# Optimization experiments

Measured on AMD Instinct MI355X. Metric: run time of the kernel, lower is better.

## Reference

```python
import jax, jax.numpy as jnp
import numpy as np

# Model hyperparameters (match init_kwargs)
K = 4          # number of experts (branches)
STEPS = 3
TOP_N = 2
HEADS = 2
DIM_HEAD = 64
ROUTE_TEMP = 1.5
C = 256        # channels


def conv3x3(x, w, b):
    # x: [B,H,W,Cin], w: [3,3,Cin,Cout], b: [Cout]
    y = jax.lax.conv_general_dilated(
        x, w, window_strides=(1, 1), padding='SAME',
        dimension_numbers=('NHWC', 'HWIO', 'NHWC'))
    return y + b


def setup_inputs() -> dict:
    key = jax.random.key(0)
    ks = jax.random.split(key, 8)
    B, H, W = 32, 32, 32
    D = HEADS * DIM_HEAD  # 128
    glorot = jax.nn.initializers.glorot_uniform()
    x = jax.random.normal(ks[0], (B, H, W, C), dtype=jnp.float32)
    q = glorot(ks[1], (HEADS, DIM_HEAD), jnp.float32)          # router queries
    Wk = glorot(ks[2], (C, D), jnp.float32)                    # 1x1 conv key proj
    Wv = glorot(ks[3], (C, D), jnp.float32)                    # 1x1 conv val proj
    Wmlp = glorot(ks[4], (D, K), jnp.float32)                  # head_mlp (mlp_hidden=0)
    alpha = jnp.zeros((), jnp.float32)                         # attn_log_alpha
    We = glorot(ks[5], (K * 3, 3, C, C), jnp.float32).reshape(K, 3, 3, C, C)
    be = jnp.zeros((K, C), jnp.float32)
    return {"x": x, "q": q, "Wk": Wk, "Wv": Wv, "Wmlp": Wmlp,
            "alpha": alpha, "We": We, "be": be}


def reference(x, q, Wk, Wv, Wmlp, alpha, We, be):
    B, H, W, Cc = x.shape
    S = H * W
    allowed = jnp.ones((B, K), x.dtype)
    last_oh = jax.nn.one_hot(jnp.full((B,), K - 1), K, dtype=x.dtype)
    scale = jnp.asarray(S, x.dtype)
    a = jax.nn.softplus(alpha)

    for t in range(STEPS):
        # ---- AttnPoolRouter ----
        k = jnp.einsum('bhwc,cd->bhwd', x, Wk).reshape(B, S, HEADS, DIM_HEAD)
        v = jnp.einsum('bhwc,cd->bhwd', x, Wv).reshape(B, S, HEADS, DIM_HEAD)
        # attention logits: [B, heads, S]
        attn = jax.nn.softmax(
            jnp.einsum('nd,bsnd->bns', q, k) / jnp.sqrt(jnp.asarray(DIM_HEAD, x.dtype)),
            axis=-1)
        pooled = jnp.einsum('bns,bsnd->bnd', attn, v).reshape(B, HEADS * DIM_HEAD)
        logits = pooled @ Wmlp                                   # [B, K]
        attn_map = attn.mean(axis=1).reshape(B, H, W, 1)

        # ---- routing with exclusion mask ----
        masked_logits = jnp.where(allowed > 0.5, logits, jnp.asarray(-1e9, x.dtype))
        weights = jax.nn.softmax(masked_logits / ROUTE_TEMP, axis=-1)
        top_vals, top_idx = jax.lax.top_k(weights, TOP_N)        # [B, n]
        mask_oh = jax.nn.one_hot(top_idx, K, dtype=x.dtype).sum(axis=1)  # [B, K]
        wm = weights * mask_oh
        wsel = wm / (wm.sum(axis=-1, keepdims=True) + 1e-9)      # == straight-through fwd value

        # ---- modulate input and run selected experts (dense-equivalent) ----
        x_mod = x * (1.0 + attn_map * scale * a)
        y = jnp.zeros_like(x)
        for e in range(K):
            ye = conv3x3(x_mod, We[e], be[e])
            y = y + wsel[:, e][:, None, None, None] * ye

        # ---- update allowed: disallow step top-1 unless it's the last expert ----
        top1 = top_idx[:, 0]
        not_last = (top1 != K - 1).astype(x.dtype)
        delta = jax.nn.one_hot(top1, K, dtype=x.dtype) * not_last[:, None]
        allowed = jnp.clip(allowed - delta, 0.0, 1.0)
        allowed = jnp.maximum(allowed, last_oh)
        x = y
    return x
```

## Files before the change

kernel.cpp:

```cpp
#include <hip/hip_runtime.h>

typedef _Float16 f16x8 __attribute__((ext_vector_type(8)));
typedef __fp16 fp16x2 __attribute__((ext_vector_type(2)));
typedef __attribute__((ext_vector_type(4))) float f32x4;

#define CC 256
#define SS 1024
#define KK 4
#define XR 6
#define XC 34
#define NCELL (XR * XC)

__device__ __forceinline__ unsigned int pk2h(float a, float b) {
  fp16x2 h = __builtin_amdgcn_cvt_pkrtz(a, b);
  return __builtin_bit_cast(unsigned int, h);
}

__device__ __forceinline__ void gll16(const void* g, void* l) {
  __builtin_amdgcn_global_load_lds((const __attribute__((address_space(1))) void*)g,
                                   (__attribute__((address_space(3))) void*)l, 16, 0, 0);
}

#define S_VMCNT0 asm volatile("s_waitcnt vmcnt(0)" ::: "memory")
#define S_LGKM0 asm volatile("s_waitcnt lgkmcnt(0)" ::: "memory")
#define SCHED0 __builtin_amdgcn_sched_barrier(0)

__global__ void qk_kernel(const float* __restrict__ Wk, const float* __restrict__ q,
                          float* __restrict__ qk) {
  int t = blockIdx.x * blockDim.x + threadIdx.x;
  if (t >= CC * 2) return;
  int c = t >> 1, n = t & 1;
  float s = 0.f;
  for (int d = 0; d < 64; ++d) s += Wk[c * 128 + n * 64 + d] * q[n * 64 + d];
  qk[c * 2 + n] = s;
}

__global__ void poolpart_kernel(const float* __restrict__ x, const float* __restrict__ qk,
                                float* __restrict__ scores, float* __restrict__ part) {
  __shared__ float xs[64][260];
  __shared__ float ds[2][64];
  __shared__ float qks[512];
  int ch = blockIdx.x, b = blockIdx.y, tid = threadIdx.x;
  int s0 = ch * 64;
  const float* xb = x + ((size_t)b * 1024 + s0) * 256;
  for (int i = tid; i < 4096; i += 256) {
    int r = i >> 6, c4 = (i & 63) << 2;
    *(float4*)(&xs[r][c4]) = *(const float4*)(xb + (size_t)r * 256 + c4);
  }
  for (int i = tid; i < 512; i += 256) qks[i] = qk[i];
  __syncthreads();

  int p = tid >> 2, qd = tid & 3;
  float d0 = 0.f, d1 = 0.f;
  const float* xr = &xs[p][qd];
  const float* qr = qks + 2 * qd;
#pragma unroll 8
  for (int j = 0; j < 64; ++j) {
    float xv = xr[4 * j];
    d0 += xv * qr[8 * j];
    d1 += xv * qr[8 * j + 1];
  }
  d0 += __shfl_xor(d0, 1, 64); d0 += __shfl_xor(d0, 2, 64);
  d1 += __shfl_xor(d1, 1, 64); d1 += __shfl_xor(d1, 2, 64);
  if (qd == 0) {
    ds[0][p] = d0 * 0.125f;
    ds[1][p] = d1 * 0.125f;
    scores[((size_t)b * 2 + 0) * 1024 + s0 + p] = d0 * 0.125f;
    scores[((size_t)b * 2 + 1) * 1024 + s0 + p] = d1 * 0.125f;
  }
  __syncthreads();

  int lane = tid & 63, wv = tid >> 6;
  if (wv < 2) {
    float v = ds[wv][lane];
    float m = v;
#pragma unroll
    for (int sh = 32; sh >= 1; sh >>= 1) m = fmaxf(m, __shfl_xor(m, sh, 64));
    float e = expf(v - m);
    float Z = e;
#pragma unroll
    for (int sh = 32; sh >= 1; sh >>= 1) Z += __shfl_xor(Z, sh, 64);
    ds[wv][lane] = e;
    if (lane == 0) {
      float* o = part + ((size_t)(b * 16 + ch)) * 520;
      o[wv] = m;
      o[2 + wv] = Z;
    }
  }
  __syncthreads();
  float a0a = 0.f, a0b = 0.f, a0c = 0.f, a0d = 0.f;
  float a1a = 0.f, a1b = 0.f, a1c = 0.f, a1d = 0.f;
#pragma unroll 4
  for (int s4 = 0; s4 < 16; ++s4) {
    float x0 = xs[s4 * 4 + 0][tid];
    float x1 = xs[s4 * 4 + 1][tid];
    float x2 = xs[s4 * 4 + 2][tid];
    float x3 = xs[s4 * 4 + 3][tid];
    a0a += ds[0][s4 * 4 + 0] * x0;
    a0b += ds[0][s4 * 4 + 1] * x1;
    a0c += ds[0][s4 * 4 + 2] * x2;
    a0d += ds[0][s4 * 4 + 3] * x3;
    a1a += ds[1][s4 * 4 + 0] * x0;
    a1b += ds[1][s4 * 4 + 1] * x1;
    a1c += ds[1][s4 * 4 + 2] * x2;
    a1d += ds[1][s4 * 4 + 3] * x3;
  }
  float* o = part + ((size_t)(b * 16 + ch)) * 520;
  o[4 + tid] = (a0a + a0b) + (a0c + a0d);
  o[4 + 256 + tid] = (a1a + a1b) + (a1c + a1d);
}

__global__ void route_kernel(const float* __restrict__ part, const float* __restrict__ scores,
                             const float* __restrict__ Wv, const float* __restrict__ Wmlp,
                             const float* __restrict__ alpha, float* __restrict__ allowed,
                             float* __restrict__ rowscale,
                             int* __restrict__ selE, float* __restrict__ selW, int step) {
  __shared__ float xs[512];
  __shared__ float phalf[256];
  __shared__ float pooled[128];
  __shared__ float lg[4];
  __shared__ float Msh[2], iZsh[2];
  __shared__ float cs[2][16];
  int b = blockIdx.x, tid = threadIdx.x;
  if (tid < 2) {
    float m = -1e30f;
    for (int ch = 0; ch < 16; ++ch)
      m = fmaxf(m, part[((size_t)(b * 16 + ch)) * 520 + tid]);
    float z = 0.f;
    for (int ch = 0; ch < 16; ++ch) {
      const float* p = part + ((size_t)(b * 16 + ch)) * 520;
      z += expf(p[tid] - m) * p[2 + tid];
    }
    Msh[tid] = m;
    iZsh[tid] = 1.f / z;
  }
  __syncthreads();
  if (tid < 32) {
    int n = tid >> 4, ch = tid & 15;
    cs[n][ch] = expf(part[((size_t)(b * 16 + ch)) * 520 + n] - Msh[n]);
  }
  float M0 = Msh[0], M1 = Msh[1], iZ0 = iZsh[0], iZ1 = iZsh[1];
  {
    float al = alpha[0];
    float a = (al > 20.f) ? al : log1pf(expf(al));
    float k = 0.5f * 1024.f * a;
    for (int i = tid; i < 1024; i += 256) {
      float d0 = scores[((size_t)b * 2 + 0) * 1024 + i];
      float d1 = scores[((size_t)b * 2 + 1) * 1024 + i];
      rowscale[(size_t)b * 1024 + i] = 1.f + k * (expf(d0 - M0) * iZ0 + expf(d1 - M1) * iZ1);
    }
  }
  __syncthreads();
#pragma unroll
  for (int i = 0; i < 2; ++i) {
    int id = tid + i * 256;
    int n = id >> 8, c = id & 255;
    float s = 0.f;
    for (int ch = 0; ch < 16; ++ch)
      s += cs[n][ch] * part[((size_t)(b * 16 + ch)) * 520 + 4 + n * 256 + c];
    xs[id] = s * iZsh[n];
  }
  __syncthreads();
  {
    int d = tid & 127, half = tid >> 7;
    int n = d >> 6;
    const float* xr = xs + n * 256 + half * 128;
    const float* wv = Wv + (size_t)half * 128 * 128 + d;
    float s = 0.f;
#pragma unroll 4
    for (int c = 0; c < 128; ++c) s += xr[c] * wv[(size_t)c * 128];
    phalf[tid] = s;
  }
  __syncthreads();
  if (tid < 128) pooled[tid] = phalf[tid] + phalf[tid + 128];
  __syncthreads();
  if (tid < 4) {
    float s = 0.f;
    for (int d = 0; d < 128; ++d) s += pooled[d] * Wmlp[d * 4 + tid];
    lg[tid] = s;
  }
  __syncthreads();
  if (tid == 0) {
    float al[KK];
    if (step == 0) { for (int k = 0; k < KK; ++k) al[k] = 1.f; }
    else           { for (int k = 0; k < KK; ++k) al[k] = allowed[b * KK + k]; }
    float ml[KK];
    for (int k = 0; k < KK; ++k)
      ml[k] = (al[k] > 0.5f) ? lg[k] * (1.f / 1.5f) : (-1e9f) * (1.f / 1.5f);
    float m = ml[0];
    for (int k = 1; k < KK; ++k) m = fmaxf(m, ml[k]);
    float e[KK], ssum = 0.f;
    for (int k = 0; k < KK; ++k) { e[k] = expf(ml[k] - m); ssum += e[k]; }
    float w[KK];
    for (int k = 0; k < KK; ++k) w[k] = e[k] / ssum;
    int i0 = 0;
    for (int k = 1; k < KK; ++k) if (w[k] > w[i0]) i0 = k;
    int i1 = -1;
    for (int k = 0; k < KK; ++k) {
      if (k == i0) continue;
      if (i1 < 0 || w[k] > w[i1]) i1 = k;
    }
    float denom = w[i0] + w[i1] + 1e-9f;
    selE[b * 2 + 0] = i0;
    selE[b * 2 + 1] = i1;
    selW[b * 2 + 0] = w[i0] / denom;
    selW[b * 2 + 1] = w[i1] / denom;
    if (i0 != KK - 1) al[i0] = fminf(fmaxf(al[i0] - 1.f, 0.f), 1.f);
    al[KK - 1] = fmaxf(al[KK - 1], 1.f);
    for (int k = 0; k < KK; ++k) allowed[b * KK + k] = al[k];
  }
}

__global__ void combine_w_kernel(const float* __restrict__ We,
                                 const int* __restrict__ selE, const float* __restrict__ selW,
                                 unsigned short* __restrict__ Wc_h) {
  int tile = blockIdx.x;
  int b = blockIdx.y;
  int tap = tile >> 3, kc = tile & 7;
  int co = threadIdx.x;
  int e0 = selE[b * 2], e1 = selE[b * 2 + 1];
  float w0 = selW[b * 2], w1 = selW[b * 2 + 1];
  __shared__ float ts[32][257];
  const float* s0 = We + (size_t)(e0 * 9 + tap) * 65536 + (size_t)(kc * 32) * 256 + co;
  const float* s1 = We + (size_t)(e1 * 9 + tap) * 65536 + (size_t)(kc * 32) * 256 + co;
  for (int ci = 0; ci < 32; ++ci)
    ts[ci][co] = w0 * s0[(size_t)ci * 256] + w1 * s1[(size_t)ci * 256];
  __syncthreads();
  unsigned int hw[16];
#pragma unroll
  for (int k2 = 0; k2 < 16; ++k2) hw[k2] = pk2h(ts[k2 * 2][co], ts[k2 * 2 + 1][co]);
  size_t base = ((size_t)b * 72 + tile) * 8192 + (size_t)co * 32;
#pragma unroll
  for (int j = 0; j < 4; ++j)
    *(uint4*)(Wc_h + base + j * 8) = make_uint4(hw[j * 4], hw[j * 4 + 1], hw[j * 4 + 2], hw[j * 4 + 3]);
}

__global__ __launch_bounds__(256, 2) void conv_kernel(
    const float* __restrict__ xin, const float* __restrict__ rowscale,
    const unsigned short* __restrict__ Wc_h,
    const float* __restrict__ be,
    const int* __restrict__ selE, const float* __restrict__ selW,
    float* __restrict__ out) {
  __shared__ __align__(16) unsigned char xsB[2][NCELL * 64];
  __shared__ __align__(16) unsigned char BsB[2][3 * 8192];
  __shared__ float rs_lds[NCELL];

  int bid = blockIdx.x;
  int xcd = bid & 7, t2b = bid >> 3;
  int mt = t2b & 7, gs = t2b >> 3;
  int g = gs * 8 + xcd;
  int b = g >> 1, nt = g & 1;
  int h0 = mt * 4;
  int tid = threadIdx.x;
  int lane = tid & 63, wid = tid >> 6;
  int wm = wid >> 1, wn = wid & 1;
  int l15 = lane & 15, kl = lane >> 4;

  int e0 = selE[b * 2], e1 = selE[b * 2 + 1];
  float w0 = selW[b * 2], w1 = selW[b * 2 + 1];

  int cellb[4];
#pragma unroll
  for (int mf = 0; mf < 4; ++mf) {
    int p0 = wm * 64 + mf * 16;
    cellb[mf] = (p0 >> 5) * XC + (p0 & 31) + l15;
  }
  int bbyte[4];
#pragma unroll
  for (int nf = 0; nf < 4; ++nf) {
    int co = wn * 64 + nf * 16 + l15;
    bbyte[nf] = (co * 64 + kl * 16) ^ ((co & 7) << 4);
  }
  int elemoff[2];
#pragma unroll
  for (int j = 0; j < 2; ++j) {
    int oh = wid * 2048 + j * 1024 + lane * 16;
    int co = ((oh >> 7) << 1) | (((oh >> 6) ^ (oh >> 8)) & 1);
    int s = ((oh >> 4) & 3) ^ (co & 3);
    elemoff[j] = (nt * 128 + co) * 32 + s * 8;
  }
  const unsigned short* WH = Wc_h + (size_t)b * 72 * 8192;

  float bias[4];
#pragma unroll
  for (int nf = 0; nf < 4; ++nf) {
    int con = nt * 128 + wn * 64 + nf * 16 + l15;
    bias[nf] = w0 * be[e0 * 256 + con] + w1 * be[e1 * 256 + con];
  }

  f32x4 acc[4][4];
#pragma unroll
  for (int mf = 0; mf < 4; ++mf)
#pragma unroll
    for (int nf = 0; nf < 4; ++nf) acc[mf][nf] = (f32x4){0.f, 0.f, 0.f, 0.f};

  for (int i = tid; i < NCELL; i += 256) {
    int r = i / XC, c = i - r * XC;
    int gr = h0 - 1 + r, gc = c - 1;
    float v = 0.f;
    if (gr >= 0 && gr < 32 && gc >= 0 && gc < 32)
      v = rowscale[(size_t)b * 1024 + gr * 32 + gc];
    rs_lds[i] = v;
  }

  auto stage_x = [&](int kcc) {
    unsigned char* xd = xsB[kcc & 1];
    for (int idx = tid; idx < NCELL * 2; idx += 256) {
      int hk = (idx >= NCELL) ? 1 : 0;
      int cell = idx - hk * NCELL;
      int r = cell / XC, c = cell - r * XC;
      int gr = h0 - 1 + r, gc = c - 1;
      uint4 pk = make_uint4(0, 0, 0, 0), pk2 = make_uint4(0, 0, 0, 0);
      if (gr >= 0 && gr < 32 && gc >= 0 && gc < 32) {
        const float* src = xin + (((size_t)b * 32 + gr) * 32 + gc) * 256 + kcc * 32 + hk * 16;
        float sc = rs_lds[cell];
        float xv[16];
        *(float4*)(xv + 0) = *(const float4*)(src + 0);
        *(float4*)(xv + 4) = *(const float4*)(src + 4);
        *(float4*)(xv + 8) = *(const float4*)(src + 8);
        *(float4*)(xv + 12) = *(const float4*)(src + 12);
        unsigned int u[8];
#pragma unroll
        for (int e2 = 0; e2 < 8; ++e2)
          u[e2] = pk2h(xv[e2 * 2] * sc, xv[e2 * 2 + 1] * sc);
        pk = make_uint4(u[0], u[1], u[2], u[3]);
        pk2 = make_uint4(u[4], u[5], u[6], u[7]);
      }
      int sx = (cell & 7) << 4;
      int b0 = (cell * 64 + hk * 32) ^ sx;
      int b1 = (cell * 64 + hk * 32 + 16) ^ sx;
      *(uint4*)(xd + b0) = pk;
      *(uint4*)(xd + b1) = pk2;
    }
  };

  auto issue_group = [&](int kcA, int subBase, int buf) {
#pragma unroll
    for (int t = 0; t < 3; ++t) {
      const unsigned short* sp = WH + (size_t)((subBase + t) * 8 + kcA) * 8192;
      char* lb = (char*)&BsB[buf][t * 8192] + wid * 2048;
      gll16(sp + elemoff[0], lb);
      gll16(sp + elemoff[1], lb + 1024);
    }
    SCHED0;
  };

  auto do_tap = [&](int tap, int tIdx, const unsigned char* xsCur, int buf) {
    const int dy = (tap >= 6) ? 2 : ((tap >= 3) ? 1 : 0);
    const int dx = tap - dy * 3;
    const int dcell = dy * XC + dx;
    const unsigned char* bp = &BsB[buf][tIdx * 8192];
    f16x8 af[4], bf[4];
#pragma unroll
    for (int mf = 0; mf < 4; ++mf) {
      int cell = cellb[mf] + dcell;
      int abyte = (cell * 64 + kl * 16) ^ ((cell & 7) << 4);
      af[mf] = *(const f16x8*)(xsCur + abyte);
    }
#pragma unroll
    for (int nf = 0; nf < 4; ++nf) bf[nf] = *(const f16x8*)(bp + bbyte[nf]);
    __builtin_amdgcn_s_setprio(1);
#pragma unroll
    for (int mf = 0; mf < 4; ++mf)
#pragma unroll
      for (int nf = 0; nf < 4; ++nf)
        acc[mf][nf] = __builtin_amdgcn_mfma_f32_16x16x32_f16(af[mf], bf[nf], acc[mf][nf], 0, 0, 0);
    __builtin_amdgcn_s_setprio(0);
  };

  issue_group(0, 0, 0);
  __syncthreads();
  stage_x(0);
  S_VMCNT0;
  S_LGKM0;
  SCHED0;
  __builtin_amdgcn_s_barrier();

#pragma unroll 1
  for (int kc = 0; kc < 8; ++kc) {
    const unsigned char* xsCur = xsB[kc & 1];
    const int bX = kc & 1;
    if (kc < 7) stage_x(kc + 1);
    issue_group(kc, 3, bX ^ 1);
    do_tap(0, 0, xsCur, bX);
    do_tap(1, 1, xsCur, bX);
    do_tap(2, 2, xsCur, bX);
    S_VMCNT0;
    SCHED0;
    __builtin_amdgcn_s_barrier();
    issue_group(kc, 6, bX);
    do_tap(3, 0, xsCur, bX ^ 1);
    do_tap(4, 1, xsCur, bX ^ 1);
    do_tap(5, 2, xsCur, bX ^ 1);
    S_VMCNT0;
    SCHED0;
    __builtin_amdgcn_s_barrier();
    if (kc < 7) issue_group(kc + 1, 0, bX ^ 1);
    do_tap(6, 0, xsCur, bX);
    do_tap(7, 1, xsCur, bX);
    do_tap(8, 2, xsCur, bX);
    if (kc < 7) { S_LGKM0; }
    S_VMCNT0;
    SCHED0;
    __builtin_amdgcn_s_barrier();
  }

#pragma unroll
  for (int mf = 0; mf < 4; ++mf) {
    int p0 = wm * 64 + mf * 16;
    int pr = p0 >> 5, pc = p0 & 31;
    size_t rowbase = ((size_t)b * 32 + h0 + pr) * 32;
#pragma unroll
    for (int nf = 0; nf < 4; ++nf) {
      int co = nt * 128 + wn * 64 + nf * 16 + l15;
#pragma unroll
      for (int rr = 0; rr < 4; ++rr) {
        int col = pc + kl * 4 + rr;
        out[(rowbase + col) * 256 + co] = acc[mf][nf][rr] + bias[nf];
      }
    }
  }
}

extern "C" void kernel_launch(void* const* d_in, const int* in_sizes, int n_in,
                              void* d_out, int out_size, void* d_ws, size_t ws_size,
                              hipStream_t stream) {
  const float* x_in  = (const float*)d_in[0];
  const float* q     = (const float*)d_in[1];
  const float* Wk    = (const float*)d_in[2];
  const float* Wv    = (const float*)d_in[3];
  const float* Wmlp  = (const float*)d_in[4];
  const float* alpha = (const float*)d_in[5];
  const float* We    = (const float*)d_in[6];
  const float* be    = (const float*)d_in[7];
  float* out = (float*)d_out;
  float* ws = (float*)d_ws;

  float* qk       = ws;
  float* scores   = qk + 512;
  float* rowscale = scores + 65536;
  float* part     = rowscale + 32768;
  float* allowed  = part + 266240;
  float* selW     = allowed + 128;
  int*   selE     = (int*)(selW + 64);
  float* xbuf     = selW + 128;
  unsigned short* Wc_h = (unsigned short*)(xbuf + 8388608);

  qk_kernel<<<2, 256, 0, stream>>>(Wk, q, qk);

  const float* step_in[3] = {x_in, out, xbuf};
  float* step_out[3] = {out, xbuf, out};

  for (int t = 0; t < 3; ++t) {
    const float* xc = step_in[t];
    poolpart_kernel<<<dim3(16, 32), 256, 0, stream>>>(xc, qk, scores, part);
    route_kernel<<<32, 256, 0, stream>>>(part, scores, Wv, Wmlp, alpha, allowed, rowscale, selE, selW, t);
    combine_w_kernel<<<dim3(72, 32), 256, 0, stream>>>(We, selE, selW, Wc_h);
    conv_kernel<<<512, 256, 0, stream>>>(xc, rowscale, Wc_h, be, selE, selW, step_out[t]);
  }
}
```

Measured before the change: 290.9 us.

## Fuse per-batch expert weight combination into conv kernel via shared fp16 expert weights

Removes the per-step combine_w_kernel, which built a per-batch fp16 combined weight tensor from the fp32 expert weights. A one-time prep kernel now converts all four experts' weights to a fp16 tiled layout, and the conv kernel loads the two selected experts' tiles into registers. It combines them with packed fp16 FMA and writes the result to LDS, replacing the async global_load_lds path. This cuts per-step weight traffic and a launch, but doubles global loads inside the conv loop, adds VALU work and register pressure, and does the weighting in fp16 instead of fp32.

```diff
diff --git a/kernel.cpp b/kernel.cpp
--- a/kernel.cpp
+++ b/kernel.cpp
@@ -14,11 +14,6 @@
 __device__ __forceinline__ unsigned int pk2h(float a, float b) {
   fp16x2 h = __builtin_amdgcn_cvt_pkrtz(a, b);
   return __builtin_bit_cast(unsigned int, h);
-}
-
-__device__ __forceinline__ void gll16(const void* g, void* l) {
-  __builtin_amdgcn_global_load_lds((const __attribute__((address_space(1))) void*)g,
-                                   (__attribute__((address_space(3))) void*)l, 16, 0, 0);
 }
 
 #define S_VMCNT0 asm volatile("s_waitcnt vmcnt(0)" ::: "memory")
@@ -33,6 +28,24 @@
   float s = 0.f;
   for (int d = 0; d < 64; ++d) s += Wk[c * 128 + n * 64 + d] * q[n * 64 + d];
   qk[c * 2 + n] = s;
+}
+
+__global__ void prep_w_kernel(const float* __restrict__ We, unsigned short* __restrict__ Wt) {
+  int tile = blockIdx.x;
+  int e = blockIdx.y;
+  int tap = tile >> 3, kc = tile & 7;
+  int co = threadIdx.x;
+  __shared__ float ts[32][257];
+  const float* src = We + (size_t)(e * 9 + tap) * 65536 + (size_t)(kc * 32) * 256 + co;
+  for (int ci = 0; ci < 32; ++ci) ts[ci][co] = src[(size_t)ci * 256];
+  __syncthreads();
+  unsigned int hw[16];
+#pragma unroll
+  for (int k2 = 0; k2 < 16; ++k2) hw[k2] = pk2h(ts[k2 * 2][co], ts[k2 * 2 + 1][co]);
+  size_t base = ((size_t)e * 72 + tile) * 8192 + (size_t)co * 32;
+#pragma unroll
+  for (int j = 0; j < 4; ++j)
+    *(uint4*)(Wt + base + j * 8) = make_uint4(hw[j * 4], hw[j * 4 + 1], hw[j * 4 + 2], hw[j * 4 + 3]);
 }
 
 __global__ void poolpart_kernel(const float* __restrict__ x, const float* __restrict__ qk,
@@ -211,33 +224,9 @@
   }
 }
 
-__global__ void combine_w_kernel(const float* __restrict__ We,
-                                 const int* __restrict__ selE, const float* __restrict__ selW,
-                                 unsigned short* __restrict__ Wc_h) {
-  int tile = blockIdx.x;
-  int b = blockIdx.y;
-  int tap = tile >> 3, kc = tile & 7;
-  int co = threadIdx.x;
-  int e0 = selE[b * 2], e1 = selE[b * 2 + 1];
-  float w0 = selW[b * 2], w1 = selW[b * 2 + 1];
-  __shared__ float ts[32][257];
-  const float* s0 = We + (size_t)(e0 * 9 + tap) * 65536 + (size_t)(kc * 32) * 256 + co;
-  const float* s1 = We + (size_t)(e1 * 9 + tap) * 65536 + (size_t)(kc * 32) * 256 + co;
-  for (int ci = 0; ci < 32; ++ci)
-    ts[ci][co] = w0 * s0[(size_t)ci * 256] + w1 * s1[(size_t)ci * 256];
-  __syncthreads();
-  unsigned int hw[16];
-#pragma unroll
-  for (int k2 = 0; k2 < 16; ++k2) hw[k2] = pk2h(ts[k2 * 2][co], ts[k2 * 2 + 1][co]);
-  size_t base = ((size_t)b * 72 + tile) * 8192 + (size_t)co * 32;
-#pragma unroll
-  for (int j = 0; j < 4; ++j)
-    *(uint4*)(Wc_h + base + j * 8) = make_uint4(hw[j * 4], hw[j * 4 + 1], hw[j * 4 + 2], hw[j * 4 + 3]);
-}
-
 __global__ __launch_bounds__(256, 2) void conv_kernel(
     const float* __restrict__ xin, const float* __restrict__ rowscale,
-    const unsigned short* __restrict__ Wc_h,
+    const unsigned short* __restrict__ Wt,
     const float* __restrict__ be,
     const int* __restrict__ selE, const float* __restrict__ selW,
     float* __restrict__ out) {
@@ -258,6 +247,10 @@
 
   int e0 = selE[b * 2], e1 = selE[b * 2 + 1];
   float w0 = selW[b * 2], w1 = selW[b * 2 + 1];
+  fp16x2 w0h = {(__fp16)w0, (__fp16)w0};
+  fp16x2 w1h = {(__fp16)w1, (__fp16)w1};
+  const unsigned short* W0 = Wt + (size_t)e0 * 72 * 8192;
+  const unsigned short* W1 = Wt + (size_t)e1 * 72 * 8192;
 
   int cellb[4];
 #pragma unroll
@@ -271,15 +264,14 @@
     int co = wn * 64 + nf * 16 + l15;
     bbyte[nf] = (co * 64 + kl * 16) ^ ((co & 7) << 4);
   }
-  int elemoff[2];
-#pragma unroll
-  for (int j = 0; j < 2; ++j) {
-    int oh = wid * 2048 + j * 1024 + lane * 16;
-    int co = ((oh >> 7) << 1) | (((oh >> 6) ^ (oh >> 8)) & 1);
-    int s = ((oh >> 4) & 3) ^ (co & 3);
-    elemoff[j] = (nt * 128 + co) * 32 + s * 8;
-  }
-  const unsigned short* WH = Wc_h + (size_t)b * 72 * 8192;
+  int scol[2], sq[2], sdst[2];
+#pragma unroll
+  for (int s2 = 0; s2 < 2; ++s2) {
+    int u = tid + s2 * 256;
+    scol[s2] = u >> 2;
+    sq[s2] = u & 3;
+    sdst[s2] = (scol[s2] * 64 + sq[s2] * 16) ^ ((scol[s2] & 7) << 4);
+  }
 
   float bias[4];
 #pragma unroll
@@ -334,15 +326,38 @@
     }
   };
 
-  auto issue_group = [&](int kcA, int subBase, int buf) {
+  auto load_group = [&](int kcA, int subBase, uint4* A, uint4* B) {
 #pragma unroll
     for (int t = 0; t < 3; ++t) {
-      const unsigned short* sp = WH + (size_t)((subBase + t) * 8 + kcA) * 8192;
-      char* lb = (char*)&BsB[buf][t * 8192] + wid * 2048;
-      gll16(sp + elemoff[0], lb);
-      gll16(sp + elemoff[1], lb + 1024);
+      size_t toff = (size_t)((subBase + t) * 8 + kcA) * 8192;
+#pragma unroll
+      for (int s2 = 0; s2 < 2; ++s2) {
+        size_t off = toff + (size_t)(nt * 128 + scol[s2]) * 32 + sq[s2] * 8;
+        A[t * 2 + s2] = *(const uint4*)(W0 + off);
+        B[t * 2 + s2] = *(const uint4*)(W1 + off);
+      }
     }
     SCHED0;
+  };
+
+  auto cmb = [&](unsigned int a, unsigned int bq) -> unsigned int {
+    fp16x2 ha = __builtin_bit_cast(fp16x2, a);
+    fp16x2 hb = __builtin_bit_cast(fp16x2, bq);
+    fp16x2 hc = ha * w0h + hb * w1h;
+    return __builtin_bit_cast(unsigned int, hc);
+  };
+  auto combine_write = [&](int buf, const uint4* A, const uint4* B) {
+#pragma unroll
+    for (int t = 0; t < 3; ++t)
+#pragma unroll
+      for (int s2 = 0; s2 < 2; ++s2) {
+        uint4 a = A[t * 2 + s2], bq = B[t * 2 + s2], r;
+        r.x = cmb(a.x, bq.x);
+        r.y = cmb(a.y, bq.y);
+        r.z = cmb(a.z, bq.z);
+        r.w = cmb(a.w, bq.w);
+        *(uint4*)(&BsB[buf][t * 8192 + sdst[s2]]) = r;
+      }
   };
 
   auto do_tap = [&](int tap, int tIdx, const unsigned char* xsCur, int buf) {
@@ -368,10 +383,13 @@
     __builtin_amdgcn_s_setprio(0);
   };
 
-  issue_group(0, 0, 0);
+  uint4 LA[6], LB[6];
+  load_group(0, 0, LA, LB);
   __syncthreads();
   stage_x(0);
   S_VMCNT0;
+  SCHED0;
+  combine_write(0, LA, LB);
   S_LGKM0;
   SCHED0;
   __builtin_amdgcn_s_barrier();
@@ -381,27 +399,37 @@
     const unsigned char* xsCur = xsB[kc & 1];
     const int bX = kc & 1;
     if (kc < 7) stage_x(kc + 1);
-    issue_group(kc, 3, bX ^ 1);
+    load_group(kc, 3, LA, LB);
     do_tap(0, 0, xsCur, bX);
     do_tap(1, 1, xsCur, bX);
     do_tap(2, 2, xsCur, bX);
     S_VMCNT0;
     SCHED0;
+    combine_write(bX ^ 1, LA, LB);
+    S_LGKM0;
+    SCHED0;
     __builtin_amdgcn_s_barrier();
-    issue_group(kc, 6, bX);
+    load_group(kc, 6, LA, LB);
     do_tap(3, 0, xsCur, bX ^ 1);
     do_tap(4, 1, xsCur, bX ^ 1);
     do_tap(5, 2, xsCur, bX ^ 1);
     S_VMCNT0;
     SCHED0;
+    combine_write(bX, LA, LB);
+    S_LGKM0;
+    SCHED0;
     __builtin_amdgcn_s_barrier();
-    if (kc < 7) issue_group(kc + 1, 0, bX ^ 1);
+    if (kc < 7) load_group(kc + 1, 0, LA, LB);
     do_tap(6, 0, xsCur, bX);
     do_tap(7, 1, xsCur, bX);
     do_tap(8, 2, xsCur, bX);
-    if (kc < 7) { S_LGKM0; }
-    S_VMCNT0;
-    SCHED0;
+    if (kc < 7) {
+      S_VMCNT0;
+      SCHED0;
+      combine_write(bX ^ 1, LA, LB);
+      S_LGKM0;
+      SCHED0;
+    }
     __builtin_amdgcn_s_barrier();
   }
 
@@ -444,9 +472,10 @@
   float* selW     = allowed + 128;
   int*   selE     = (int*)(selW + 64);
   float* xbuf     = selW + 128;
-  unsigned short* Wc_h = (unsigned short*)(xbuf + 8388608);
+  unsigned short* Wt = (unsigned short*)(xbuf + 8388608);
 
   qk_kernel<<<2, 256, 0, stream>>>(Wk, q, qk);
+  prep_w_kernel<<<dim3(72, 4), 256, 0, stream>>>(We, Wt);
 
   const float* step_in[3] = {x_in, out, xbuf};
   float* step_out[3] = {out, xbuf, out};
@@ -455,7 +484,6 @@
     const float* xc = step_in[t];
     poolpart_kernel<<<dim3(16, 32), 256, 0, stream>>>(xc, qk, scores, part);
     route_kernel<<<32, 256, 0, stream>>>(part, scores, Wv, Wmlp, alpha, allowed, rowscale, selE, selW, t);
-    combine_w_kernel<<<dim3(72, 32), 256, 0, stream>>>(We, selE, selW, Wc_h);
-    conv_kernel<<<512, 256, 0, stream>>>(xc, rowscale, Wc_h, be, selE, selW, step_out[t]);
-  }
-}
+    conv_kernel<<<512, 256, 0, stream>>>(xc, rowscale, Wt, be, selE, selW, step_out[t]);
+  }
+}
```

New measurement: 260.7 us. 1.12x faster.
